# Performance work log

Measured on AMD Instinct MI355X. Metric: run time of the kernel, lower is better.

The kernel has to match this reference:

```python
import jax, jax.numpy as jnp
import numpy as np

N_EVENTS = 16
N_SAMPLES = 2 ** 15          # 32768
STEP = 256                   # window_size // 2
LONG_WINDOW = 4096
LONG_COEFFS = LONG_WINDOW // 2 + 1   # 2049
LONG_STEP = LONG_WINDOW // 2         # 2048
LONG_FRAMES = N_SAMPLES // LONG_STEP # 16
N_FRAMES = N_SAMPLES // STEP         # 128
B = 8                                 # audio batch
BE = B * N_EVENTS                     # event batch = 128


def setup_inputs() -> dict:
    key = jax.random.key(0)
    k1, k2, k3, k4 = jax.random.split(key, 4)
    env = jax.random.uniform(k1, (BE, LONG_WINDOW, LONG_FRAMES), jnp.float32)
    tf = jax.random.normal(k2, (BE, LONG_COEFFS * 2, LONG_FRAMES), jnp.float32)
    noise = jax.random.uniform(k3, (BE, LONG_WINDOW, LONG_FRAMES), jnp.float32)
    indices = jax.random.randint(k4, (B, N_EVENTS), 0, N_FRAMES, dtype=jnp.int32)
    return {"env": env, "tf": tf, "noise": noise, "indices": indices}


def _event_render(env, tf, noise):
    # env, noise: (BE, LONG_WINDOW, LONG_FRAMES); tf: (BE, 2*LONG_COEFFS, LONG_FRAMES)
    batch = env.shape[0]
    energy = env * (noise * 2.0 - 1.0)  # uniform_(-1, 1) noise scaled by amp

    # magnitude = norm over interleaved (real, imag) pairs, per torch view semantics
    pairs = tf.reshape(batch, LONG_COEFFS, 2, LONG_FRAMES)
    mag = jnp.sqrt(jnp.sum(pairs * pairs, axis=2))  # (batch, C, F)
    mx = jnp.max(mag.reshape(batch, -1), axis=-1, keepdims=True)
    mag = (mag.reshape(batch, -1) / (mx + 1e-8)).reshape(batch, LONG_COEFFS, LONG_FRAMES)
    imag = tf[:, LONG_COEFFS:, :]
    phase = jnp.arctan2(imag, mag) * np.pi  # torch.angle(complex(mag, imag)) * pi
    tfc = mag * jnp.exp(1j * phase)         # complex transfer fn (batch, C, F)

    # sequential per-frame recurrence: state feeds through rfft/irfft filtering
    e_t = jnp.transpose(energy, (2, 0, 1))  # (F, batch, W)
    t_t = jnp.transpose(tfc, (2, 0, 1))     # (F, batch, C)

    def step(prev, inp):
        e, t = inp
        local = prev + e
        spec = jnp.fft.rfft(local, axis=-1, norm='ortho') * t
        frame = jnp.fft.irfft(spec, n=LONG_WINDOW, axis=-1, norm='ortho')
        return frame, frame

    init = jnp.zeros((batch, LONG_WINDOW), energy.dtype)
    _, frames = jax.lax.scan(step, init, (e_t, t_t))   # (F, batch, W)
    frames = jnp.transpose(frames, (1, 0, 2))          # (batch, F, W)

    # overlap-add with hop = LONG_STEP = W/2: split frames into halves and add
    halves = frames.reshape(batch, LONG_FRAMES, 2, LONG_STEP)
    out = jnp.zeros((batch, LONG_FRAMES + 1, LONG_STEP), frames.dtype)
    out = out.at[:, :LONG_FRAMES].add(halves[:, :, 0])
    out = out.at[:, 1:].add(halves[:, :, 1])
    return out.reshape(batch, -1)[:, :N_SAMPLES]       # (BE, N_SAMPLES)


def _segment_render(atoms, indices):
    # atoms: (BE, N_SAMPLES) -> (B, N_EVENTS, N_SAMPLES); scatter-add at time offsets
    x = atoms.reshape(B, N_EVENTS, N_SAMPLES)
    times = indices * STEP                                      # (B, E)
    pos = times[:, :, None] + jnp.arange(N_SAMPLES)[None, None, :]  # (B, E, S)
    out = jnp.zeros((B, 2 * N_SAMPLES), x.dtype)
    bidx = jnp.arange(B)[:, None, None]
    out = out.at[bidx, pos].add(x)
    return out[:, None, :N_SAMPLES]                             # (B, 1, N_SAMPLES)


def reference(env, tf, noise, indices):
    atoms = _event_render(env, tf, noise)
    return _segment_render(atoms, indices)
```

## Files before the change

### kernel.cpp

```cpp
#include <hip/hip_runtime.h>
#include <math.h>

#define TWO_PI 6.283185307179586f

#define OFF_ET   0ull
#define OFF_E    8388608ull
#define OFF_MAXP 16781312ull

__device__ __forceinline__ int swz(int n) { return n ^ ((n >> 5) & 31); }

__device__ __forceinline__ int permf(int k) {
    return ((k & 1) << 10) | (((k >> 1) & 3) << 8) | (((k >> 3) & 3) << 6)
         | (((k >> 5) & 3) << 4) | (((k >> 7) & 3) << 2) | ((k >> 9) & 3);
}

__device__ __forceinline__ void r4_fwd(float* cr, float* ci, int j, int h, float ang) {
    int p0 = swz(j), p1 = swz(j + h), p2 = swz(j + 2 * h), p3 = swz(j + 3 * h);
    float ar = cr[p0], ai = ci[p0];
    float br = cr[p1], bi = ci[p1];
    float crr = cr[p2], cri = ci[p2];
    float drr = cr[p3], dri = ci[p3];
    float u0r = ar + crr, u0i = ai + cri;
    float u1r = ar - crr, u1i = ai - cri;
    float u2r = br + drr, u2i = bi + dri;
    float u3r = br - drr, u3i = bi - dri;
    float s1, c1; __sincosf(ang, &s1, &c1);
    float c2 = c1 * c1 - s1 * s1, s2 = 2.f * c1 * s1;
    float c3 = c1 * c2 - s1 * s2, s3 = s1 * c2 + c1 * s2;
    cr[p0] = u0r + u2r; ci[p0] = u0i + u2i;
    float z1r = u1r + u3i, z1i = u1i - u3r;
    cr[p1] = z1r * c1 + z1i * s1; ci[p1] = z1i * c1 - z1r * s1;
    float z2r = u0r - u2r, z2i = u0i - u2i;
    cr[p2] = z2r * c2 + z2i * s2; ci[p2] = z2i * c2 - z2r * s2;
    float z3r = u1r - u3i, z3i = u1i + u3r;
    cr[p3] = z3r * c3 + z3i * s3; ci[p3] = z3i * c3 - z3r * s3;
}

__device__ __forceinline__ void r4_inv(float* cr, float* ci, int j, int h, float ang) {
    int p0 = swz(j), p1 = swz(j + h), p2 = swz(j + 2 * h), p3 = swz(j + 3 * h);
    float z0r = cr[p0], z0i = ci[p0];
    float z1r = cr[p1], z1i = ci[p1];
    float z2r = cr[p2], z2i = ci[p2];
    float z3r = cr[p3], z3i = ci[p3];
    float s1, c1; __sincosf(ang, &s1, &c1);
    float c2 = c1 * c1 - s1 * s1, s2 = 2.f * c1 * s1;
    float c3 = c1 * c2 - s1 * s2, s3 = s1 * c2 + c1 * s2;
    float t1r = z1r * c1 - z1i * s1, t1i = z1i * c1 + z1r * s1;
    float t2r = z2r * c2 - z2i * s2, t2i = z2i * c2 + z2r * s2;
    float t3r = z3r * c3 - z3i * s3, t3i = z3i * c3 + z3r * s3;
    float u0r = z0r + t2r, u0i = z0i + t2i;
    float u1r = z0r - t2r, u1i = z0i - t2i;
    float u2r = t1r + t3r, u2i = t1i + t3i;
    float u3r = t1r - t3r, u3i = t1i - t3i;
    cr[p0] = u0r + u2r; ci[p0] = u0i + u2i;
    cr[p1] = u1r - u3i; ci[p1] = u1i + u3r;
    cr[p2] = u0r - u2r; ci[p2] = u0i - u2i;
    cr[p3] = u1r + u3i; ci[p3] = u1i - u3r;
}

__global__ __launch_bounds__(256) void k_prep(const float* __restrict__ env,
                                              const float* __restrict__ noise,
                                              const float* __restrict__ tf,
                                              float* __restrict__ ws) {
    __shared__ float tile[256][17];
    int tid = threadIdx.x;
    if (blockIdx.x < 2048) {
        int be = blockIdx.x >> 4;
        int n0 = (blockIdx.x & 15) << 8;
        size_t base = (size_t)be * 65536 + (size_t)n0 * 16;
        float* eT = ws + OFF_ET;
#pragma unroll
        for (int j = 0; j < 16; ++j) {
            int i = tid + j * 256;
            float e = env[base + i];
            float nz = noise[base + i];
            tile[i >> 4][i & 15] = e * (nz * 2.0f - 1.0f);
        }
        __syncthreads();
#pragma unroll
        for (int f = 0; f < 16; ++f)
            eT[(size_t)(be * 16 + f) * 4096 + n0 + tid] = tile[tid][f];
    } else {
        int bb = blockIdx.x - 2048;
        int be = bb >> 3;
        int chunk = bb & 7;
        const float* tfb = tf + (size_t)be * 65568;
        float* red = &tile[0][0];
        int start = chunk * 4098, end = start + 4098;
        float mx = 0.f;
        for (int i = start + tid; i < end; i += 256) {
            int c = i >> 4, f = i & 15;
            float a = tfb[c * 32 + f];
            float b = tfb[c * 32 + 16 + f];
            mx = fmaxf(mx, a * a + b * b);
        }
        red[tid] = mx;
        __syncthreads();
        for (int s = 128; s > 0; s >>= 1) {
            if (tid < s) red[tid] = fmaxf(red[tid], red[tid + s]);
            __syncthreads();
        }
        if (tid == 0) ws[OFF_MAXP + bb] = red[0];
    }
}

__global__ __launch_bounds__(512) void k_fft_fwd(float* __restrict__ ws) {
    __shared__ float cr[2048], ci[2048];
    int tid = threadIdx.x;
    int be = blockIdx.x >> 4, f = blockIdx.x & 15;
    const float4* src = (const float4*)(ws + OFF_ET) + (size_t)(be * 16 + f) * 1024;
#pragma unroll
    for (int it = 0; it < 2; ++it) {
        int idx = tid + it * 512;
        float4 v = src[idx];
        int n0 = idx * 2;
        cr[swz(n0)] = v.x;     ci[swz(n0)] = v.y;
        cr[swz(n0 + 1)] = v.z; ci[swz(n0 + 1)] = v.w;
    }
    __syncthreads();
#pragma unroll
    for (int it = 0; it < 2; ++it) {
        int i = tid + it * 512;
        int sj = swz(i), sjb = swz(i + 1024);
        float ar = cr[sj], ai = ci[sj], br = cr[sjb], bi = ci[sjb];
        float dr = ar - br, di = ai - bi;
        float s, c; __sincosf((float)i * (TWO_PI / 2048.0f), &s, &c);
        cr[sj] = ar + br; ci[sj] = ai + bi;
        cr[sjb] = dr * c + di * s; ci[sjb] = di * c - dr * s;
    }
    __syncthreads();
    r4_fwd(cr, ci, (tid >> 8) * 1024 + (tid & 255), 256, (float)(tid & 255) * (TWO_PI / 1024.0f)); __syncthreads();
    r4_fwd(cr, ci, (tid >> 6) * 256 + (tid & 63), 64, (float)(tid & 63) * (TWO_PI / 256.0f)); __syncthreads();
    r4_fwd(cr, ci, (tid & 31) * 64 + (tid >> 5), 16, (float)(tid >> 5) * (TWO_PI / 64.0f)); __syncthreads();
    r4_fwd(cr, ci, (tid & 127) * 16 + (tid >> 7), 4, (float)(tid >> 7) * (TWO_PI / 16.0f)); __syncthreads();
    r4_fwd(cr, ci, tid * 4, 1, 0.0f); __syncthreads();
    float2* Eg = (float2*)(ws + OFF_E) + (size_t)(be * 16 + f) * 2049;
    for (int k = tid; k <= 1024; k += 512) {
        int pk = swz(permf(k));
        int pm = swz(permf((2048 - k) & 2047));
        float zkr = cr[pk], zki = ci[pk], zmr = cr[pm], zmi = ci[pm];
        float xer = 0.5f * (zkr + zmr), xei = 0.5f * (zki - zmi);
        float xor_ = 0.5f * (zki + zmi), xoi = 0.5f * (zmr - zkr);
        float s4, c4; __sincosf((float)k * (TWO_PI / 4096.0f), &s4, &c4);
        float wr = xor_ * c4 + xoi * s4;
        float wi = xoi * c4 - xor_ * s4;
        Eg[k] = make_float2(xer + wr, xei + wi);
        Eg[2048 - k] = make_float2(xer - wr, wi - xei);
    }
}

__global__ __launch_bounds__(256) void k_recur(const float* __restrict__ tf,
                                               float* __restrict__ ws) {
    __shared__ float sm2[256 * 17];
    __shared__ float sim[256 * 17];
    int tid = threadIdx.x;
    int be = blockIdx.y;
    int k0 = blockIdx.x << 8;
    int nk = 2049 - k0; if (nk > 256) nk = 256;
    const float* tfb = tf + (size_t)be * 65568;
    const float4* ab4 = (const float4*)tfb;
    const float4* im4 = (const float4*)(tfb + 32784);

    for (int u = tid; u < nk * 4; u += 256) {
        int g = u >> 2, e = u & 3;
        float4 A = ab4[(k0 + g) * 8 + e];
        float4 Bv = ab4[(k0 + g) * 8 + e + 4];
        float4 I = im4[(k0 + g) * 4 + e];
        int o = g * 17 + e * 4;
        sm2[o + 0] = A.x * A.x + Bv.x * Bv.x;
        sm2[o + 1] = A.y * A.y + Bv.y * Bv.y;
        sm2[o + 2] = A.z * A.z + Bv.z * Bv.z;
        sm2[o + 3] = A.w * A.w + Bv.w * Bv.w;
        sim[o + 0] = I.x; sim[o + 1] = I.y; sim[o + 2] = I.z; sim[o + 3] = I.w;
    }
    __syncthreads();

    if (tid >= nk) return;
    int kg = k0 + tid;
    const float* mp = ws + OFF_MAXP + be * 8;
    float m2x = fmaxf(fmaxf(fmaxf(mp[0], mp[1]), fmaxf(mp[2], mp[3])),
                      fmaxf(fmaxf(mp[4], mp[5]), fmaxf(mp[6], mp[7])));
    float rden = 1.0f / (sqrtf(m2x) + 1e-8f);
    float2* Eg = (float2*)(ws + OFF_E) + (size_t)be * 16 * 2049 + kg;
    float2 ev[16];
#pragma unroll
    for (int f = 0; f < 16; ++f) ev[f] = Eg[(size_t)f * 2049];
    float ym = (kg == 0 || kg == 2048) ? 0.0f : 1.0f;
    float sr = 0.f, si = 0.f;
#pragma unroll
    for (int f = 0; f < 16; ++f) {
        float mh = sqrtf(sm2[tid * 17 + f]) * rden;
        float ph = atan2f(sim[tid * 17 + f], mh) * 3.14159265358979f;
        float sp, cp; __sincosf(ph, &sp, &cp);
        float Tr = mh * cp, Ti = mh * sp;
        si *= ym;
        sr += ev[f].x; si += ev[f].y;
        float nr = sr * Tr - si * Ti;
        si = sr * Ti + si * Tr;
        sr = nr;
        Eg[(size_t)f * 2049] = make_float2(sr, si);
    }
}

__global__ __launch_bounds__(512) void k_fft_inv(float* __restrict__ ws) {
    __shared__ float cr[2048], ci[2048];
    int tid = threadIdx.x;
    int be = blockIdx.x >> 4, f = blockIdx.x & 15;
    const float2* Yg = (const float2*)(ws + OFF_E) + (size_t)(be * 16 + f) * 2049;
    const float SCL = 1.0f / 2048.0f;
    for (int k = tid; k <= 1024; k += 512) {
        float2 Yk = Yg[k];
        float2 Ym = Yg[2048 - k];
        if (k == 0) {
            float y0 = Yk.x * SCL, yn = Ym.x * SCL;
            cr[swz(0)] = 0.5f * (y0 + yn);
            ci[swz(0)] = 0.5f * (y0 - yn);
        } else {
            float ykr = Yk.x * SCL, yki = Yk.y * SCL;
            float ymr = Ym.x * SCL, ymi = Ym.y * SCL;
            float er = 0.5f * (ykr + ymr), ei = 0.5f * (yki - ymi);
            float dr = ykr - ymr, di = yki + ymi;
            float s4, c4; __sincosf((float)k * (TWO_PI / 4096.0f), &s4, &c4);
            float orr = 0.5f * (dr * c4 - di * s4);
            float oi = 0.5f * (dr * s4 + di * c4);
            int pk = swz(permf(k)), pm = swz(permf(2048 - k));
            cr[pk] = er - oi; ci[pk] = ei + orr;
            cr[pm] = er + oi; ci[pm] = orr - ei;
        }
    }
    __syncthreads();
    r4_inv(cr, ci, tid * 4, 1, 0.0f); __syncthreads();
    r4_inv(cr, ci, (tid & 127) * 16 + (tid >> 7), 4, (float)(tid >> 7) * (TWO_PI / 16.0f)); __syncthreads();
    r4_inv(cr, ci, (tid & 31) * 64 + (tid >> 5), 16, (float)(tid >> 5) * (TWO_PI / 64.0f)); __syncthreads();
    r4_inv(cr, ci, (tid >> 6) * 256 + (tid & 63), 64, (float)(tid & 63) * (TWO_PI / 256.0f)); __syncthreads();
    r4_inv(cr, ci, (tid >> 8) * 1024 + (tid & 255), 256, (float)(tid & 255) * (TWO_PI / 1024.0f)); __syncthreads();
#pragma unroll
    for (int it = 0; it < 2; ++it) {
        int i = tid + it * 512;
        int sj = swz(i), sjb = swz(i + 1024);
        float s, c; __sincosf((float)i * (TWO_PI / 2048.0f), &s, &c);
        float br = cr[sjb], bi = ci[sjb];
        float tr = br * c - bi * s, ti2 = br * s + bi * c;
        float ar = cr[sj], ai = ci[sj];
        cr[sj] = ar + tr;  ci[sj] = ai + ti2;
        cr[sjb] = ar - tr; ci[sjb] = ai - ti2;
    }
    __syncthreads();
    float2* Fg = (float2*)(ws + OFF_ET) + (size_t)(be * 16 + f) * 2048;
#pragma unroll
    for (int it = 0; it < 4; ++it) {
        int m = tid + it * 512;
        Fg[m] = make_float2(cr[swz(m)], ci[swz(m)]);
    }
}

__global__ __launch_bounds__(256) void k_segment(const float* __restrict__ ws,
                                                 const int* __restrict__ indices,
                                                 float* __restrict__ out) {
    int gid = blockIdx.x * 256 + threadIdx.x;
    int b = gid >> 13;
    int t = (gid & 8191) << 2;
    const float* F = ws + OFF_ET;
    float4 acc = make_float4(0.f, 0.f, 0.f, 0.f);
#pragma unroll
    for (int e = 0; e < 16; ++e) {
        int te = indices[b * 16 + e] * 256;
        if (t >= te) {
            int d = t - te;
            int j = d >> 11, r = d & 2047;
            size_t base = (size_t)(b * 16 + e) * 65536;
            float4 v = *(const float4*)(F + base + j * 4096 + r);
            acc.x += v.x; acc.y += v.y; acc.z += v.z; acc.w += v.w;
            if (j >= 1) {
                float4 w = *(const float4*)(F + base + (j - 1) * 4096 + 2048 + r);
                acc.x += w.x; acc.y += w.y; acc.z += w.z; acc.w += w.w;
            }
        }
    }
    ((float4*)out)[gid] = acc;
}

extern "C" void kernel_launch(void* const* d_in, const int* in_sizes, int n_in,
                              void* d_out, int out_size, void* d_ws, size_t ws_size,
                              hipStream_t stream) {
    const float* env = (const float*)d_in[0];
    const float* tf = (const float*)d_in[1];
    const float* noise = (const float*)d_in[2];
    const int* indices = (const int*)d_in[3];
    float* ws = (float*)d_ws;
    float* out = (float*)d_out;

    k_prep<<<dim3(3072), dim3(256), 0, stream>>>(env, noise, tf, ws);
    k_fft_fwd<<<dim3(2048), dim3(512), 0, stream>>>(ws);
    k_recur<<<dim3(9, 128), dim3(256), 0, stream>>>(tf, ws);
    k_fft_inv<<<dim3(2048), dim3(512), 0, stream>>>(ws);
    k_segment<<<dim3(256), dim3(256), 0, stream>>>(ws, indices, out);
}
```

Measured before the change: 91.66 us.

## Fuse inverse real-FFT pre-twiddle into recurrence kernel and cache indices in shared memory

The recurrence kernel now handles each bin k together with its mirror 2048-k. It applies the inverse real-to-complex packing twiddle and scaling directly and writes a packed 2048-point complex buffer. The inverse FFT kernel then only loads contiguous float4 pairs and permutes them, with no per-bin twiddle and no mirrored gather. Grid and work per thread change (4 blocks per event, two bins per thread, Nyquist bin handled by a single thread). The segment kernel moves event offsets into shared memory via a 2D grid. This adds an extra workspace region and a serial 16-step tail for bin 1024 in one thread per event.

```diff
diff --git a/kernel.cpp b/kernel.cpp
--- a/kernel.cpp
+++ b/kernel.cpp
@@ -6,6 +6,7 @@
 #define OFF_ET   0ull
 #define OFF_E    8388608ull
 #define OFF_MAXP 16781312ull
+#define OFF_Z    16782336ull
 
 __device__ __forceinline__ int swz(int n) { return n ^ ((n >> 5) & 31); }
 
@@ -151,54 +152,103 @@
 
 __global__ __launch_bounds__(256) void k_recur(const float* __restrict__ tf,
                                                float* __restrict__ ws) {
-    __shared__ float sm2[256 * 17];
-    __shared__ float sim[256 * 17];
+    __shared__ float sm2lo[256 * 17], simlo[256 * 17];
+    __shared__ float sm2hi[256 * 17], simhi[256 * 17];
     int tid = threadIdx.x;
     int be = blockIdx.y;
     int k0 = blockIdx.x << 8;
-    int nk = 2049 - k0; if (nk > 256) nk = 256;
+    int hi0 = 1793 - k0;
     const float* tfb = tf + (size_t)be * 65568;
     const float4* ab4 = (const float4*)tfb;
     const float4* im4 = (const float4*)(tfb + 32784);
 
-    for (int u = tid; u < nk * 4; u += 256) {
-        int g = u >> 2, e = u & 3;
-        float4 A = ab4[(k0 + g) * 8 + e];
-        float4 Bv = ab4[(k0 + g) * 8 + e + 4];
-        float4 I = im4[(k0 + g) * 4 + e];
+    for (int u = tid; u < 2048; u += 256) {
+        int half = u >> 10, v = u & 1023;
+        int g = v >> 2, e = v & 3;
+        int bin = half ? (hi0 + g) : (k0 + g);
+        float4 A = ab4[bin * 8 + e];
+        float4 Bv = ab4[bin * 8 + e + 4];
+        float4 I = im4[bin * 4 + e];
         int o = g * 17 + e * 4;
-        sm2[o + 0] = A.x * A.x + Bv.x * Bv.x;
-        sm2[o + 1] = A.y * A.y + Bv.y * Bv.y;
-        sm2[o + 2] = A.z * A.z + Bv.z * Bv.z;
-        sm2[o + 3] = A.w * A.w + Bv.w * Bv.w;
-        sim[o + 0] = I.x; sim[o + 1] = I.y; sim[o + 2] = I.z; sim[o + 3] = I.w;
-    }
-    __syncthreads();
-
-    if (tid >= nk) return;
-    int kg = k0 + tid;
+        float* sm = half ? sm2hi : sm2lo;
+        float* si = half ? simhi : simlo;
+        sm[o + 0] = A.x * A.x + Bv.x * Bv.x;
+        sm[o + 1] = A.y * A.y + Bv.y * Bv.y;
+        sm[o + 2] = A.z * A.z + Bv.z * Bv.z;
+        sm[o + 3] = A.w * A.w + Bv.w * Bv.w;
+        si[o + 0] = I.x; si[o + 1] = I.y; si[o + 2] = I.z; si[o + 3] = I.w;
+    }
+    __syncthreads();
+
+    int k = k0 + tid;
+    int m = 2048 - k;
+    int rhi = 255 - tid;
     const float* mp = ws + OFF_MAXP + be * 8;
     float m2x = fmaxf(fmaxf(fmaxf(mp[0], mp[1]), fmaxf(mp[2], mp[3])),
                       fmaxf(fmaxf(mp[4], mp[5]), fmaxf(mp[6], mp[7])));
     float rden = 1.0f / (sqrtf(m2x) + 1e-8f);
-    float2* Eg = (float2*)(ws + OFF_E) + (size_t)be * 16 * 2049 + kg;
-    float2 ev[16];
-#pragma unroll
-    for (int f = 0; f < 16; ++f) ev[f] = Eg[(size_t)f * 2049];
-    float ym = (kg == 0 || kg == 2048) ? 0.0f : 1.0f;
-    float sr = 0.f, si = 0.f;
+    const float2* Eb = (const float2*)(ws + OFF_E) + (size_t)be * 16 * 2049;
+    float2* Zb = (float2*)(ws + OFF_Z) + (size_t)be * 16 * 2048;
+    float2 evlo[16], evhi[16];
 #pragma unroll
     for (int f = 0; f < 16; ++f) {
-        float mh = sqrtf(sm2[tid * 17 + f]) * rden;
-        float ph = atan2f(sim[tid * 17 + f], mh) * 3.14159265358979f;
+        evlo[f] = Eb[(size_t)f * 2049 + k];
+        evhi[f] = Eb[(size_t)f * 2049 + m];
+    }
+    float ym = (k == 0) ? 0.0f : 1.0f;
+    float s4, c4; __sincosf((float)k * (TWO_PI / 4096.0f), &s4, &c4);
+    const float SCL = 1.0f / 2048.0f;
+    float srl = 0.f, sil = 0.f, srh = 0.f, sih = 0.f;
+#pragma unroll
+    for (int f = 0; f < 16; ++f) {
+        float mh = sqrtf(sm2lo[tid * 17 + f]) * rden;
+        float ph = atan2f(simlo[tid * 17 + f], mh) * 3.14159265358979f;
         float sp, cp; __sincosf(ph, &sp, &cp);
         float Tr = mh * cp, Ti = mh * sp;
-        si *= ym;
-        sr += ev[f].x; si += ev[f].y;
-        float nr = sr * Tr - si * Ti;
-        si = sr * Ti + si * Tr;
-        sr = nr;
-        Eg[(size_t)f * 2049] = make_float2(sr, si);
+        sil *= ym;
+        srl += evlo[f].x; sil += evlo[f].y;
+        float nr = srl * Tr - sil * Ti;
+        sil = srl * Ti + sil * Tr; srl = nr;
+        float mh2 = sqrtf(sm2hi[rhi * 17 + f]) * rden;
+        float ph2 = atan2f(simhi[rhi * 17 + f], mh2) * 3.14159265358979f;
+        float sp2, cp2; __sincosf(ph2, &sp2, &cp2);
+        float Tr2 = mh2 * cp2, Ti2 = mh2 * sp2;
+        sih *= ym;
+        srh += evhi[f].x; sih += evhi[f].y;
+        float nr2 = srh * Tr2 - sih * Ti2;
+        sih = srh * Ti2 + sih * Tr2; srh = nr2;
+        float2* Zf = Zb + (size_t)f * 2048;
+        if (k == 0) {
+            float y0 = srl * SCL, yn = srh * SCL;
+            Zf[0] = make_float2(0.5f * (y0 + yn), 0.5f * (y0 - yn));
+        } else {
+            float ykr = srl * SCL, yki = sil * SCL;
+            float ymr = srh * SCL, ymi = sih * SCL;
+            float er = 0.5f * (ykr + ymr), ei = 0.5f * (yki - ymi);
+            float dr = ykr - ymr, di = yki + ymi;
+            float orr = 0.5f * (dr * c4 - di * s4);
+            float oi = 0.5f * (dr * s4 + di * c4);
+            Zf[k] = make_float2(er - oi, ei + orr);
+            Zf[m] = make_float2(er + oi, orr - ei);
+        }
+    }
+    if (k0 == 0 && tid == 0) {
+        float sr = 0.f, si = 0.f;
+#pragma unroll
+        for (int f = 0; f < 16; ++f) {
+            float a = tfb[1024 * 32 + f];
+            float b = tfb[1024 * 32 + 16 + f];
+            float im = tfb[32784 + 1024 * 16 + f];
+            float mh = sqrtf(a * a + b * b) * rden;
+            float ph = atan2f(im, mh) * 3.14159265358979f;
+            float sp, cp; __sincosf(ph, &sp, &cp);
+            float Tr = mh * cp, Ti = mh * sp;
+            float2 e = Eb[(size_t)f * 2049 + 1024];
+            sr += e.x; si += e.y;
+            float nr = sr * Tr - si * Ti;
+            si = sr * Ti + si * Tr; sr = nr;
+            Zb[(size_t)f * 2048 + 1024] = make_float2(sr * SCL, -si * SCL);
+        }
     }
 }
 
@@ -206,27 +256,15 @@
     __shared__ float cr[2048], ci[2048];
     int tid = threadIdx.x;
     int be = blockIdx.x >> 4, f = blockIdx.x & 15;
-    const float2* Yg = (const float2*)(ws + OFF_E) + (size_t)(be * 16 + f) * 2049;
-    const float SCL = 1.0f / 2048.0f;
-    for (int k = tid; k <= 1024; k += 512) {
-        float2 Yk = Yg[k];
-        float2 Ym = Yg[2048 - k];
-        if (k == 0) {
-            float y0 = Yk.x * SCL, yn = Ym.x * SCL;
-            cr[swz(0)] = 0.5f * (y0 + yn);
-            ci[swz(0)] = 0.5f * (y0 - yn);
-        } else {
-            float ykr = Yk.x * SCL, yki = Yk.y * SCL;
-            float ymr = Ym.x * SCL, ymi = Ym.y * SCL;
-            float er = 0.5f * (ykr + ymr), ei = 0.5f * (yki - ymi);
-            float dr = ykr - ymr, di = yki + ymi;
-            float s4, c4; __sincosf((float)k * (TWO_PI / 4096.0f), &s4, &c4);
-            float orr = 0.5f * (dr * c4 - di * s4);
-            float oi = 0.5f * (dr * s4 + di * c4);
-            int pk = swz(permf(k)), pm = swz(permf(2048 - k));
-            cr[pk] = er - oi; ci[pk] = ei + orr;
-            cr[pm] = er + oi; ci[pm] = orr - ei;
-        }
+    const float4* Zg = (const float4*)((float2*)(ws + OFF_Z) + (size_t)(be * 16 + f) * 2048);
+#pragma unroll
+    for (int it = 0; it < 2; ++it) {
+        int idx = tid + it * 512;
+        float4 v = Zg[idx];
+        int n0 = idx * 2;
+        int p0 = swz(permf(n0)), p1 = swz(permf(n0 + 1));
+        cr[p0] = v.x; ci[p0] = v.y;
+        cr[p1] = v.z; ci[p1] = v.w;
     }
     __syncthreads();
     r4_inv(cr, ci, tid * 4, 1, 0.0f); __syncthreads();
@@ -257,14 +295,18 @@
 __global__ __launch_bounds__(256) void k_segment(const float* __restrict__ ws,
                                                  const int* __restrict__ indices,
                                                  float* __restrict__ out) {
-    int gid = blockIdx.x * 256 + threadIdx.x;
-    int b = gid >> 13;
-    int t = (gid & 8191) << 2;
+    __shared__ int ste[16];
+    int tid = threadIdx.x;
+    int b = blockIdx.y;
+    if (tid < 16) ste[tid] = indices[b * 16 + tid] * 256;
+    __syncthreads();
+    int g = blockIdx.x * 256 + tid;
+    int t = g << 2;
     const float* F = ws + OFF_ET;
     float4 acc = make_float4(0.f, 0.f, 0.f, 0.f);
 #pragma unroll
     for (int e = 0; e < 16; ++e) {
-        int te = indices[b * 16 + e] * 256;
+        int te = ste[e];
         if (t >= te) {
             int d = t - te;
             int j = d >> 11, r = d & 2047;
@@ -277,7 +319,7 @@
             }
         }
     }
-    ((float4*)out)[gid] = acc;
+    ((float4*)out)[(size_t)b * 8192 + g] = acc;
 }
 
 extern "C" void kernel_launch(void* const* d_in, const int* in_sizes, int n_in,
@@ -292,7 +334,7 @@
 
     k_prep<<<dim3(3072), dim3(256), 0, stream>>>(env, noise, tf, ws);
     k_fft_fwd<<<dim3(2048), dim3(512), 0, stream>>>(ws);
-    k_recur<<<dim3(9, 128), dim3(256), 0, stream>>>(tf, ws);
+    k_recur<<<dim3(4, 128), dim3(256), 0, stream>>>(tf, ws);
     k_fft_inv<<<dim3(2048), dim3(512), 0, stream>>>(ws);
-    k_segment<<<dim3(256), dim3(256), 0, stream>>>(ws, indices, out);
-}
+    k_segment<<<dim3(32, 8), dim3(256), 0, stream>>>(ws, indices, out);
+}
```

Result: no change. 93.28 us (+1.8%).
